# Kernel optimization log

Measured on AMD Instinct MI355X. Metric: run time of the kernel, lower is better.

Reference implementation:

```python
import jax, jax.numpy as jnp
import numpy as np

D_MODEL = 256
HIDDEN = 64
R = 1            # corr_radius
MAX_DELTA = 4.0  # max_delta_px
GROUPS = 8       # _gn_groups(64)
B, H, W = 2, 128, 128


def grid_sample_border(img, grid):
    """Bilinear grid_sample, padding_mode='border', align_corners=False.
    img: [B,C,H,W], grid: [B,Hg,Wg,2] (x,y in [-1,1]-ish). -> [B,C,Hg,Wg]"""
    Bi, C, Hi, Wi = img.shape
    x = (grid[..., 0] + 1.0) * (Wi * 0.5) - 0.5
    y = (grid[..., 1] + 1.0) * (Hi * 0.5) - 0.5
    x = jnp.clip(x, 0.0, Wi - 1.0)
    y = jnp.clip(y, 0.0, Hi - 1.0)
    x0 = jnp.floor(x); y0 = jnp.floor(y)
    wx = (x - x0)[:, None]; wy = (y - y0)[:, None]
    x0i = x0.astype(jnp.int32); y0i = y0.astype(jnp.int32)
    x1i = jnp.minimum(x0i + 1, Wi - 1); y1i = jnp.minimum(y0i + 1, Hi - 1)
    imgf = img.reshape(Bi, C, Hi * Wi)
    def gat(im, yi, xi):  # im [C,HW], yi/xi [Hg,Wg]
        return im[:, (yi * Wi + xi).reshape(-1)].reshape(C, *yi.shape)
    g = jax.vmap(gat)
    v00 = g(imgf, y0i, x0i); v01 = g(imgf, y0i, x1i)
    v10 = g(imgf, y1i, x0i); v11 = g(imgf, y1i, x1i)
    return (v00 * (1 - wx) * (1 - wy) + v01 * wx * (1 - wy)
            + v10 * (1 - wx) * wy + v11 * wx * wy)


def l2norm(x, axis):
    n = jnp.sqrt(jnp.sum(x * x, axis=axis, keepdims=True))
    return x / jnp.maximum(n, 1e-12)


def conv2d(x, w, pad):
    return jax.lax.conv_general_dilated(x, w, (1, 1), [(pad, pad), (pad, pad)],
                                        dimension_numbers=('NCHW', 'OIHW', 'NCHW'))


def group_norm(x, gamma, beta, groups=GROUPS, eps=1e-5):
    Bi, C, Hi, Wi = x.shape
    xg = x.reshape(Bi, groups, C // groups, Hi, Wi)
    mu = xg.mean(axis=(2, 3, 4), keepdims=True)
    var = xg.var(axis=(2, 3, 4), keepdims=True)
    xn = ((xg - mu) * jax.lax.rsqrt(var + eps)).reshape(Bi, C, Hi, Wi)
    return xn * gamma[None, :, None, None] + beta[None, :, None, None]


def conv_gn_gelu(x, w, g, b, pad):
    return jax.nn.gelu(group_norm(conv2d(x, w, pad), g, b), approximate=False)


def make_grid(h, w):
    xs = (jnp.arange(w, dtype=jnp.float32) + 0.5) * (2.0 / w) - 1.0
    ys = (jnp.arange(h, dtype=jnp.float32) + 0.5) * (2.0 / h) - 1.0
    gx, gy = jnp.meshgrid(xs, ys, indexing='xy')
    return jnp.stack([gx, gy], axis=-1)[None]  # [1,H,W,2]


def setup_inputs() -> dict:
    key = jax.random.key(0)
    ks = jax.random.split(key, 12)
    in_ch = D_MODEL * 3 + 2 + 1 + (2 * R + 1) ** 2  # 780
    def w(k, o, i, kh, kw):
        return (jax.random.normal(k, (o, i, kh, kw), jnp.float32)
                / np.sqrt(i * kh * kw).astype(np.float32))
    return {
        'feat_A_map': jax.random.normal(ks[0], (B, D_MODEL, H, W), jnp.float32),
        'feat_B_map': jax.random.normal(ks[1], (B, D_MODEL, H, W), jnp.float32),
        'coarse_warp': jax.random.uniform(ks[2], (B, H, W, 2), jnp.float32, -1.0, 1.0),
        'confidence': jax.random.uniform(ks[3], (B, H, W), jnp.float32),
        'enc1_w': w(ks[4], HIDDEN, in_ch, 1, 1),
        'gn1_g': jnp.ones(HIDDEN, jnp.float32), 'gn1_b': jnp.zeros(HIDDEN, jnp.float32),
        'enc2_w': w(ks[5], HIDDEN, HIDDEN, 3, 3),
        'gn2_g': jnp.ones(HIDDEN, jnp.float32), 'gn2_b': jnp.zeros(HIDDEN, jnp.float32),
        'enc3_w': w(ks[6], HIDDEN, HIDDEN, 3, 3),
        'gn3_g': jnp.ones(HIDDEN, jnp.float32), 'gn3_b': jnp.zeros(HIDDEN, jnp.float32),
        'delta_w': w(ks[7], 2, HIDDEN, 3, 3) * 0.01, 'delta_b': jnp.zeros(2, jnp.float32),
        'conf_w': w(ks[8], 1, HIDDEN, 3, 3) * 0.01, 'conf_b': jnp.zeros(1, jnp.float32),
    }


def reference(feat_A_map, feat_B_map, coarse_warp, confidence,
              enc1_w, gn1_g, gn1_b, enc2_w, gn2_g, gn2_b, enc3_w, gn3_g, gn3_b,
              delta_w, delta_b, conf_w, conf_b):
    cw = jnp.clip(jnp.nan_to_num(coarse_warp, nan=0.0, posinf=1.5, neginf=-1.5), -1.5, 1.5)
    route = jax.lax.stop_gradient(cw)  # detached routing warp
    warped_B = grid_sample_border(feat_B_map, route)
    src = make_grid(H, W)
    disp = jnp.transpose(cw - src, (0, 3, 1, 2))  # [B,2,H,W]
    conf = jnp.clip(jnp.nan_to_num(confidence, nan=0.0, posinf=1.0, neginf=0.0), 0.0, 1.0)
    conf_chw = conf[:, None]
    # warp-aware correlation over (2R+1)^2 offsets, vectorized via vmap
    fa_n = l2norm(jnp.nan_to_num(feat_A_map, nan=0.0, posinf=0.0, neginf=0.0), axis=1)
    fb = jnp.nan_to_num(feat_B_map, nan=0.0, posinf=0.0, neginf=0.0)
    offs = jnp.asarray([[2.0 * dx / W, 2.0 * dy / H]
                        for dy in range(-R, R + 1) for dx in range(-R, R + 1)],
                       dtype=jnp.float32)  # [K,2]
    grids = jnp.clip(jnp.nan_to_num(route[None] + offs[:, None, None, None, :],
                                    nan=0.0, posinf=1.5, neginf=-1.5), -1.5, 1.5)
    sampled = jax.vmap(grid_sample_border, in_axes=(None, 0))(fb, grids)  # [K,B,C,H,W]
    corr = jnp.transpose(jnp.sum(fa_n[None] * l2norm(sampled, axis=2), axis=2),
                         (1, 0, 2, 3))  # [B,K,H,W]
    x = jnp.concatenate([feat_A_map, warped_B, jnp.abs(feat_A_map - warped_B),
                         disp, conf_chw, corr], axis=1)
    h = conv_gn_gelu(x, enc1_w, gn1_g, gn1_b, 0)
    h = conv_gn_gelu(h, enc2_w, gn2_g, gn2_b, 1)
    h = conv_gn_gelu(h, enc3_w, gn3_g, gn3_b, 1)
    delta_raw = jnp.transpose(jnp.tanh(conv2d(h, delta_w, 1)
                                       + delta_b[None, :, None, None]), (0, 2, 3, 1))
    scale = jnp.asarray([2.0 * MAX_DELTA / W, 2.0 * MAX_DELTA / H], jnp.float32)
    fine_warp = jnp.clip(jnp.nan_to_num(route + delta_raw * scale,
                                        nan=0.0, posinf=1.5, neginf=-1.5), -1.5, 1.5)
    conf_delta = (conv2d(h, conf_w, 1) + conf_b[None, :, None, None])[:, 0]
    p = jnp.clip(conf, 1e-4, 1.0 - 1e-4)
    base_logit = jnp.log(p) - jnp.log1p(-p)
    refined_logits = base_logit + 0.5 * conf_delta
    refined_conf = jnp.clip(jax.nn.sigmoid(refined_logits), 0.0, 1.0)
    return (fine_warp, refined_conf, refined_logits)
```

## Files before the change

kernel.cpp:

```cpp
#include <hip/hip_runtime.h>
#include <hip/hip_bf16.h>
#include <math.h>

#define B_ 2
#define H_ 128
#define W_ 128
#define C_ 256
#define HID 64
#define PIX_PER (H_*W_)
#define NPIX (B_*PIX_PER)
#define K1STEPS 25
#define K3STEPS 18

using f32x4 = __attribute__((ext_vector_type(4))) float;
using s16x8 = __attribute__((ext_vector_type(8))) short;
using u16x2 = __attribute__((ext_vector_type(2))) unsigned short;
using u16x4 = __attribute__((ext_vector_type(4))) unsigned short;
using u16x8 = __attribute__((ext_vector_type(8))) unsigned short;

__device__ __forceinline__ float bf2f(unsigned short u) {
    return __uint_as_float(((unsigned)u) << 16);
}
__device__ __forceinline__ unsigned short f2bf(float f) {
    unsigned u = __float_as_uint(f);
    u += 0x7FFFu + ((u >> 16) & 1u);
    return (unsigned short)(u >> 16);
}
__device__ __forceinline__ float clean15(float v) {
    if (v != v) v = 0.f;
    return fminf(fmaxf(v, -1.5f), 1.5f);
}
__device__ __forceinline__ float clean01(float v) {
    if (v != v) v = 0.f;
    return fminf(fmaxf(v, 0.f), 1.f);
}

__global__ __launch_bounds__(256) void k_transpose(const float* __restrict__ A,
                                                   const float* __restrict__ Bm,
                                                   unsigned short* __restrict__ faT,
                                                   unsigned short* __restrict__ fbT)
{
    __shared__ float tile[32][33];
    int hw0 = blockIdx.x * 32;
    int c0  = blockIdx.y * 32;
    int z   = blockIdx.z;
    int b   = z >> 1;
    const float* src = (z & 1) ? Bm : A;
    unsigned short* dst = (z & 1) ? fbT : faT;
    int tx = threadIdx.x & 31, ty = threadIdx.x >> 5;
    const float* s = src + ((size_t)b * C_ + c0) * (size_t)PIX_PER + hw0;
#pragma unroll
    for (int i = 0; i < 32; i += 8) {
        float v = s[(size_t)(ty + i) * PIX_PER + tx];
        if (!isfinite(v)) v = 0.f;
        tile[ty + i][tx] = v;
    }
    __syncthreads();
    unsigned short* d = dst + ((size_t)b * PIX_PER + hw0) * C_ + c0;
#pragma unroll
    for (int i = 0; i < 32; i += 8) {
        int hwl = ty + i;
        u16x2 o;
        o[0] = f2bf(tile[2 * tx][hwl]);
        o[1] = f2bf(tile[2 * tx + 1][hwl]);
        *(u16x2*)(d + (size_t)hwl * C_ + 2 * tx) = o;
    }
}

__global__ __launch_bounds__(256) void k_pack(const float* __restrict__ w1,
                                              const float* __restrict__ w2,
                                              const float* __restrict__ w3,
                                              unsigned short* __restrict__ p1,
                                              unsigned short* __restrict__ p2,
                                              unsigned short* __restrict__ p3)
{
    int t = blockIdx.x * 256 + threadIdx.x;
    if (t < 6400) {
        int lane = t & 63, nt = (t >> 6) & 3, ks = t >> 8;
        int n = nt * 16 + (lane & 15);
        int kb = ks * 32 + 8 * (lane >> 4);
#pragma unroll
        for (int j = 0; j < 8; j++) {
            int k = kb + j;
            p1[(size_t)t * 8 + j] = (k < 780) ? f2bf(w1[(size_t)n * 780 + k]) : (unsigned short)0;
        }
    } else if (t < 6400 + 2 * 4608) {
        int which = (t - 6400) / 4608;
        int idx = (t - 6400) % 4608;
        const float* w = which ? w3 : w2;
        unsigned short* p = which ? p3 : p2;
        int lane = idx & 63, nt = (idx >> 6) & 3, ks = idx >> 8;
        int n = nt * 16 + (lane & 15);
        int tap = ks >> 1;
        int ky = tap / 3, kx = tap % 3;
#pragma unroll
        for (int j = 0; j < 8; j++) {
            int c = (ks & 1) * 32 + 8 * (lane >> 4) + j;
            p[(size_t)idx * 8 + j] = f2bf(w[(((size_t)n * 64 + c) * 3 + ky) * 3 + kx]);
        }
    }
}

__global__ __launch_bounds__(256, 4) void k_sample(const float* __restrict__ cw,
                                                   const float* __restrict__ confp,
                                                   const unsigned short* __restrict__ faT,
                                                   const unsigned short* __restrict__ fbT,
                                                   unsigned short* __restrict__ wbbuf,
                                                   unsigned short* __restrict__ tail)
{
    int wid = (blockIdx.x * 256 + threadIdx.x) >> 6;
    int lane = threadIdx.x & 63;
    int b = wid >> 14, y = (wid >> 7) & 127, x = wid & 127;

    float gx = clean15(cw[(size_t)wid * 2 + 0]);
    float gy = clean15(cw[(size_t)wid * 2 + 1]);

    float pxu = (gx + 1.f) * 64.f - 0.5f;
    float pyu = (gy + 1.f) * 64.f - 0.5f;
    float x0f = floorf(pxu), y0f = floorf(pyu);
    float wx = pxu - x0f, wy = pyu - y0f;
    int x0 = (int)x0f, y0 = (int)y0f;
    int cx[4], cy[4];
#pragma unroll
    for (int k = 0; k < 4; k++) {
        cx[k] = min(max(x0 - 1 + k, 0), 127);
        cy[k] = min(max(y0 - 1 + k, 0), 127);
    }

    const unsigned short* fbB = fbT + (size_t)b * PIX_PER * C_ + lane * 4;
    u16x4 tp[4][4];
#pragma unroll
    for (int m = 0; m < 4; m++)
#pragma unroll
        for (int k = 0; k < 4; k++)
            tp[m][k] = *(const u16x4*)(fbB + (size_t)(cy[m] * 128 + cx[k]) * C_);

    float fa[4], fa2 = 0.f;
    {
        u16x4 v = *(const u16x4*)(faT + (size_t)wid * C_ + lane * 4);
#pragma unroll
        for (int i = 0; i < 4; i++) { fa[i] = bf2f(v[i]); fa2 += fa[i] * fa[i]; }
    }

    float A[4][3], P[4][3], Q[3][3], rxp[3][4], wbv[4];
#pragma unroll
    for (int r = 0; r < 4; r++) {
        float rx[3][4];
#pragma unroll
        for (int dx = 0; dx < 3; dx++)
#pragma unroll
            for (int i = 0; i < 4; i++) {
                float t0 = bf2f(tp[r][dx][i]);
                float t1 = bf2f(tp[r][dx + 1][i]);
                rx[dx][i] = t0 + wx * (t1 - t0);
            }
#pragma unroll
        for (int dx = 0; dx < 3; dx++) {
            float a = 0.f, p = 0.f;
#pragma unroll
            for (int i = 0; i < 4; i++) { a += fa[i] * rx[dx][i]; p += rx[dx][i] * rx[dx][i]; }
            A[r][dx] = a; P[r][dx] = p;
            if (r > 0) {
                float q = 0.f;
#pragma unroll
                for (int i = 0; i < 4; i++) q += rxp[dx][i] * rx[dx][i];
                Q[r - 1][dx] = q;
            }
        }
        if (r == 1) {
#pragma unroll
            for (int i = 0; i < 4; i++) wbv[i] = rx[1][i];
        }
        if (r == 2) {
#pragma unroll
            for (int i = 0; i < 4; i++) wbv[i] += wy * (rx[1][i] - wbv[i]);
        }
        if (r < 3) {
#pragma unroll
            for (int dx = 0; dx < 3; dx++)
#pragma unroll
                for (int i = 0; i < 4; i++) rxp[dx][i] = rx[dx][i];
        }
    }

    u16x4 wbo;
#pragma unroll
    for (int i = 0; i < 4; i++) wbo[i] = f2bf(wbv[i]);
    *(u16x4*)(wbbuf + (size_t)wid * C_ + lane * 4) = wbo;

    float red[19];
    float u0 = (1.f - wy) * (1.f - wy), u1 = 2.f * wy * (1.f - wy), u2 = wy * wy;
#pragma unroll
    for (int j = 0; j < 9; j++) {
        int dy = j / 3, dx = j % 3;
        red[j]     = A[dy][dx] + wy * (A[dy + 1][dx] - A[dy][dx]);
        red[9 + j] = u0 * P[dy][dx] + u1 * Q[dy][dx] + u2 * P[dy + 1][dx];
    }
    red[18] = fa2;
#pragma unroll
    for (int m = 1; m < 64; m <<= 1)
#pragma unroll
        for (int j = 0; j < 19; j++)
            red[j] += __shfl_xor(red[j], m);

    if (lane == 0) {
        float conf = clean01(confp[wid]);
        float inv_na = rsqrtf(fmaxf(red[18], 1e-24f));
        float srcx = ((float)x + 0.5f) * 0.015625f - 1.f;
        float srcy = ((float)y + 0.5f) * 0.015625f - 1.f;
        u16x8 t0, t1, tz;
        t0[0] = f2bf(gx - srcx);
        t0[1] = f2bf(gy - srcy);
        t0[2] = f2bf(conf);
#pragma unroll
        for (int j = 0; j < 5; j++)
            t0[3 + j] = f2bf(red[j] * inv_na * rsqrtf(fmaxf(red[9 + j], 1e-24f)));
#pragma unroll
        for (int j = 0; j < 4; j++)
            t1[j] = f2bf(red[5 + j] * inv_na * rsqrtf(fmaxf(red[14 + j], 1e-24f)));
#pragma unroll
        for (int j = 4; j < 8; j++) t1[j] = 0;
#pragma unroll
        for (int j = 0; j < 8; j++) tz[j] = 0;
        unsigned short* tr = tail + (size_t)wid * 32;
        *(u16x8*)(tr)      = t0;
        *(u16x8*)(tr + 8)  = t1;
        *(u16x8*)(tr + 16) = tz;
        *(u16x8*)(tr + 24) = tz;
    }
}

__device__ __forceinline__ void gn_epilogue(const f32x4 acc[4], float* lds,
                                            float* __restrict__ pbuf, int bid,
                                            int la, int lb, int wv)
{
    int d = la >> 3;
    int slot = wv * 32 + lb * 8 + (la & 7);
#pragma unroll
    for (int nt = 0; nt < 4; nt++) {
        float s  = acc[nt][0] + acc[nt][1] + acc[nt][2] + acc[nt][3];
        float s2 = acc[nt][0] * acc[nt][0] + acc[nt][1] * acc[nt][1]
                 + acc[nt][2] * acc[nt][2] + acc[nt][3] * acc[nt][3];
        int g = nt * 2 + d;
        lds[(g * 128 + slot) * 2 + 0] = s;
        lds[(g * 128 + slot) * 2 + 1] = s2;
    }
    __syncthreads();
    int tid = threadIdx.x;
    int g = tid >> 5, i = tid & 31;
    float s  = lds[(g * 128 + i) * 2]     + lds[(g * 128 + i + 32) * 2]
             + lds[(g * 128 + i + 64) * 2] + lds[(g * 128 + i + 96) * 2];
    float s2 = lds[(g * 128 + i) * 2 + 1]     + lds[(g * 128 + i + 32) * 2 + 1]
             + lds[(g * 128 + i + 64) * 2 + 1] + lds[(g * 128 + i + 96) * 2 + 1];
#pragma unroll
    for (int m = 1; m < 32; m <<= 1) { s += __shfl_xor(s, m); s2 += __shfl_xor(s2, m); }
    if (i == 0) {
        pbuf[(bid * 8 + g) * 2]     = s;
        pbuf[(bid * 8 + g) * 2 + 1] = s2;
    }
}

__global__ __launch_bounds__(256) void k_gemm1(const unsigned short* __restrict__ faT,
                                               const unsigned short* __restrict__ wbbuf,
                                               const unsigned short* __restrict__ tail,
                                               const unsigned short* __restrict__ pack,
                                               unsigned short* __restrict__ hpre,
                                               float* __restrict__ pbuf)
{
    __shared__ float lds[8 * 128 * 2];
    int wave = (blockIdx.x * 256 + threadIdx.x) >> 6;
    int lane = threadIdx.x & 63;
    int la = lane & 15, lb = lane >> 4;
    int row = wave * 16 + la;
    const unsigned short* fa_row = faT   + (size_t)row * C_ + lb * 8;
    const unsigned short* wb_row = wbbuf + (size_t)row * C_ + lb * 8;
    f32x4 acc[4] = {{0,0,0,0},{0,0,0,0},{0,0,0,0},{0,0,0,0}};

#pragma unroll
    for (int ks = 0; ks < 8; ks++) {
        s16x8 a = *(const s16x8*)(fa_row + ks * 32);
#pragma unroll
        for (int nt = 0; nt < 4; nt++)
            acc[nt] = __builtin_amdgcn_mfma_f32_16x16x32_bf16(a,
                *(const s16x8*)(pack + ((size_t)(ks * 4 + nt) * 64 + lane) * 8), acc[nt], 0, 0, 0);
    }
#pragma unroll
    for (int ks = 0; ks < 8; ks++) {
        s16x8 a = *(const s16x8*)(wb_row + ks * 32);
#pragma unroll
        for (int nt = 0; nt < 4; nt++)
            acc[nt] = __builtin_amdgcn_mfma_f32_16x16x32_bf16(a,
                *(const s16x8*)(pack + ((size_t)((ks + 8) * 4 + nt) * 64 + lane) * 8), acc[nt], 0, 0, 0);
    }
#pragma unroll
    for (int ks = 0; ks < 8; ks++) {
        u16x8 av = *(const u16x8*)(fa_row + ks * 32);
        u16x8 bv = *(const u16x8*)(wb_row + ks * 32);
        s16x8 a;
#pragma unroll
        for (int j = 0; j < 8; j++)
            a[j] = (short)f2bf(fabsf(bf2f(av[j]) - bf2f(bv[j])));
#pragma unroll
        for (int nt = 0; nt < 4; nt++)
            acc[nt] = __builtin_amdgcn_mfma_f32_16x16x32_bf16(a,
                *(const s16x8*)(pack + ((size_t)((ks + 16) * 4 + nt) * 64 + lane) * 8), acc[nt], 0, 0, 0);
    }
    {
        s16x8 a = *(const s16x8*)(tail + (size_t)row * 32 + lb * 8);
#pragma unroll
        for (int nt = 0; nt < 4; nt++)
            acc[nt] = __builtin_amdgcn_mfma_f32_16x16x32_bf16(a,
                *(const s16x8*)(pack + ((size_t)(24 * 4 + nt) * 64 + lane) * 8), acc[nt], 0, 0, 0);
    }

    int orow = wave * 16 + lb * 4;
#pragma unroll
    for (int nt = 0; nt < 4; nt++)
#pragma unroll
        for (int r = 0; r < 4; r++)
            hpre[(size_t)(orow + r) * HID + nt * 16 + la] = f2bf(acc[nt][r]);

    gn_epilogue(acc, lds, pbuf, blockIdx.x, la, lb, (threadIdx.x >> 6));
}

__global__ __launch_bounds__(256) void k_conv3(const unsigned short* __restrict__ hin,
                                               const unsigned short* __restrict__ pack,
                                               unsigned short* __restrict__ hpre,
                                               float* __restrict__ pbuf)
{
    __shared__ float lds[8 * 128 * 2];
    int wave = (blockIdx.x * 256 + threadIdx.x) >> 6;
    int lane = threadIdx.x & 63;
    int la = lane & 15, lb = lane >> 4;
    int b = wave >> 10, y = (wave >> 3) & 127, xb = (wave & 7) * 16;
    int xx = xb + la;
    f32x4 acc[4] = {{0,0,0,0},{0,0,0,0},{0,0,0,0},{0,0,0,0}};
#pragma unroll
    for (int ks = 0; ks < K3STEPS; ks++) {
        int tap = ks >> 1;
        int yy = y + tap / 3 - 1;
        int xq = xx + tap % 3 - 1;
        s16x8 a = {0,0,0,0,0,0,0,0};
        if ((unsigned)yy < 128u && (unsigned)xq < 128u)
            a = *(const s16x8*)(hin + ((size_t)((b * 128 + yy) * 128 + xq)) * HID
                                + (ks & 1) * 32 + lb * 8);
#pragma unroll
        for (int nt = 0; nt < 4; nt++)
            acc[nt] = __builtin_amdgcn_mfma_f32_16x16x32_bf16(a,
                *(const s16x8*)(pack + ((size_t)(ks * 4 + nt) * 64 + lane) * 8), acc[nt], 0, 0, 0);
    }
    int orow = wave * 16 + lb * 4;
#pragma unroll
    for (int nt = 0; nt < 4; nt++)
#pragma unroll
        for (int r = 0; r < 4; r++)
            hpre[(size_t)(orow + r) * HID + nt * 16 + la] = f2bf(acc[nt][r]);

    gn_epilogue(acc, lds, pbuf, blockIdx.x, la, lb, (threadIdx.x >> 6));
}

__global__ __launch_bounds__(256) void k_gnapply(const unsigned short* __restrict__ hpre,
                                                 const float* __restrict__ gamma,
                                                 const float* __restrict__ beta,
                                                 const float* __restrict__ pbuf,
                                                 unsigned short* __restrict__ hn)
{
    int pix0 = blockIdx.x * 32;
    int b = pix0 >> 14;
    __shared__ float sm[16];
    {
        int g = threadIdx.x >> 5, i = threadIdx.x & 31;
        float s = 0.f, s2 = 0.f;
#pragma unroll
        for (int k = 0; k < 8; k++) {
            int bid = b * 256 + i + k * 32;
            s  += pbuf[(bid * 8 + g) * 2];
            s2 += pbuf[(bid * 8 + g) * 2 + 1];
        }
#pragma unroll
        for (int m = 1; m < 32; m <<= 1) { s += __shfl_xor(s, m); s2 += __shfl_xor(s2, m); }
        if (i == 0) {
            const float inv = 1.f / 131072.f;
            float mean = s * inv;
            float var = fmaxf(s2 * inv - mean * mean, 0.f);
            sm[g * 2] = mean;
            sm[g * 2 + 1] = rsqrtf(var + 1e-5f);
        }
    }
    __syncthreads();
    int t = blockIdx.x * 256 + threadIdx.x;
    int pix = t >> 3, g = t & 7;
    float mean = sm[g * 2], rstd = sm[g * 2 + 1];
    u16x8 v = *(const u16x8*)(hpre + (size_t)pix * HID + g * 8);
    u16x8 o;
#pragma unroll
    for (int i = 0; i < 8; i++) {
        int c = g * 8 + i;
        float xn = (bf2f(v[i]) - mean) * rstd * gamma[c] + beta[c];
        float ge = 0.5f * xn * (1.f + erff(xn * 0.70710678118654752f));
        o[i] = f2bf(ge);
    }
    *(u16x8*)(hn + (size_t)pix * HID + g * 8) = o;
}

__global__ __launch_bounds__(256) void k_final(const unsigned short* __restrict__ hn,
                                               const float* __restrict__ cw,
                                               const float* __restrict__ confp,
                                               const float* __restrict__ dw,
                                               const float* __restrict__ db,
                                               const float* __restrict__ cwgt,
                                               const float* __restrict__ cb,
                                               float* __restrict__ out)
{
    __shared__ float wds[1154];
    __shared__ float wcs[577];
    int tid = threadIdx.x;
    for (int i = tid; i < 1152; i += 256) wds[i] = dw[i];
    for (int i = tid; i < 576; i += 256) wcs[i] = cwgt[i];
    if (tid == 0) { wds[1152] = db[0]; wds[1153] = db[1]; wcs[576] = cb[0]; }
    __syncthreads();

    int t = blockIdx.x * 256 + tid;
    int pix = t >> 3, part = t & 7;
    int b = pix >> 14, y = (pix >> 7) & 127, x = pix & 127;

    float d0 = 0.f, d1 = 0.f, c0 = 0.f;
#pragma unroll
    for (int ky = 0; ky < 3; ky++) {
        int yy = y + ky - 1;
        if ((unsigned)yy >= 128u) continue;
#pragma unroll
        for (int kx = 0; kx < 3; kx++) {
            int xq = x + kx - 1;
            if ((unsigned)xq >= 128u) continue;
            const unsigned short* hp = hn + (size_t)((b * 128 + yy) * 128 + xq) * HID + part * 8;
            int widx = ky * 3 + kx;
            u16x8 v = *(const u16x8*)hp;
#pragma unroll
            for (int i = 0; i < 8; i++) {
                float f = bf2f(v[i]);
                int c = part * 8 + i;
                d0 += f * wds[c * 9 + widx];
                d1 += f * wds[576 + c * 9 + widx];
                c0 += f * wcs[c * 9 + widx];
            }
        }
    }
#pragma unroll
    for (int m = 1; m < 8; m <<= 1) {
        d0 += __shfl_xor(d0, m);
        d1 += __shfl_xor(d1, m);
        c0 += __shfl_xor(c0, m);
    }
    if (part == 0) {
        d0 = tanhf(d0 + wds[1152]);
        d1 = tanhf(d1 + wds[1153]);
        c0 += wcs[576];

        float gx = clean15(cw[(size_t)pix * 2 + 0]);
        float gy = clean15(cw[(size_t)pix * 2 + 1]);
        float fwx = fminf(fmaxf(gx + d0 * 0.0625f, -1.5f), 1.5f);
        float fwy = fminf(fmaxf(gy + d1 * 0.0625f, -1.5f), 1.5f);

        float conf = clean01(confp[pix]);
        float p = fminf(fmaxf(conf, 1e-4f), 1.f - 1e-4f);
        float bl = logf(p) - log1pf(-p);
        float rl = bl + 0.5f * c0;
        float rc = fminf(fmaxf(1.f / (1.f + expf(-rl)), 0.f), 1.f);

        out[(size_t)pix * 2 + 0] = fwx;
        out[(size_t)pix * 2 + 1] = fwy;
        out[(size_t)NPIX * 2 + pix] = rc;
        out[(size_t)NPIX * 2 + NPIX + pix] = rl;
    }
}

extern "C" void kernel_launch(void* const* d_in, const int* in_sizes, int n_in,
                              void* d_out, int out_size, void* d_ws, size_t ws_size,
                              hipStream_t stream)
{
    const float* feat_A = (const float*)d_in[0];
    const float* feat_B = (const float*)d_in[1];
    const float* cw     = (const float*)d_in[2];
    const float* conf   = (const float*)d_in[3];
    const float* w1     = (const float*)d_in[4];
    const float* g1     = (const float*)d_in[5];
    const float* b1     = (const float*)d_in[6];
    const float* w2     = (const float*)d_in[7];
    const float* g2     = (const float*)d_in[8];
    const float* b2     = (const float*)d_in[9];
    const float* w3     = (const float*)d_in[10];
    const float* g3     = (const float*)d_in[11];
    const float* b3     = (const float*)d_in[12];
    const float* dw     = (const float*)d_in[13];
    const float* db     = (const float*)d_in[14];
    const float* cwgt   = (const float*)d_in[15];
    const float* cb     = (const float*)d_in[16];
    float* out = (float*)d_out;

    char* w = (char*)d_ws;
    size_t o = 0;
    unsigned short* faT  = (unsigned short*)(w + o); o += (size_t)NPIX * C_ * 2;
    unsigned short* fbT  = (unsigned short*)(w + o); o += (size_t)NPIX * C_ * 2;
    unsigned short* wbb  = (unsigned short*)(w + o); o += (size_t)NPIX * C_ * 2;
    unsigned short* tail = (unsigned short*)(w + o); o += (size_t)NPIX * 32 * 2;
    unsigned short* hpre = (unsigned short*)(w + o); o += (size_t)NPIX * HID * 2;
    unsigned short* hnA  = (unsigned short*)(w + o); o += (size_t)NPIX * HID * 2;
    unsigned short* hnB  = (unsigned short*)(w + o); o += (size_t)NPIX * HID * 2;
    unsigned short* p1   = (unsigned short*)(w + o); o += (size_t)K1STEPS * 4 * 64 * 8 * 2;
    unsigned short* p2   = (unsigned short*)(w + o); o += (size_t)K3STEPS * 4 * 64 * 8 * 2;
    unsigned short* p3   = (unsigned short*)(w + o); o += (size_t)K3STEPS * 4 * 64 * 8 * 2;
    float* pbuf = (float*)(w + o);

    k_transpose<<<dim3(PIX_PER / 32, C_ / 32, 4), 256, 0, stream>>>(feat_A, feat_B, faT, fbT);
    k_pack<<<61, 256, 0, stream>>>(w1, w2, w3, p1, p2, p3);
    k_sample<<<NPIX / 4, 256, 0, stream>>>(cw, conf, faT, fbT, wbb, tail);

    k_gemm1<<<(NPIX / 16) / 4, 256, 0, stream>>>(faT, wbb, tail, p1, hpre, pbuf);
    k_gnapply<<<NPIX / 32, 256, 0, stream>>>(hpre, g1, b1, pbuf, hnA);

    k_conv3<<<(NPIX / 16) / 4, 256, 0, stream>>>(hnA, p2, hpre, pbuf);
    k_gnapply<<<NPIX / 32, 256, 0, stream>>>(hpre, g2, b2, pbuf, hnB);

    k_conv3<<<(NPIX / 16) / 4, 256, 0, stream>>>(hnB, p3, hpre, pbuf);
    k_gnapply<<<NPIX / 32, 256, 0, stream>>>(hpre, g3, b3, pbuf, hnA);

    k_final<<<NPIX * 8 / 256, 256, 0, stream>>>(hnA, cw, conf, dw, db, cwgt, cb, out);
}
```

Measured before the change: 151.7 us.

## Process two pixels per wave in k_sample with 16-byte loads and packed math

k_sample now assigns each pixel to a half-wave of 32 lanes instead of a full 64-lane wave, so each lane handles 8 channels through 16-byte loads instead of 4 channels through 8-byte loads. The bilinear interpolation and dot products use float2 vectors so the compiler can emit packed FP32 ops. Taps are loaded one row at a time to limit register pressure, and the shuffle reduction drops one step. The grid is halved and the occupancy hint in launch_bounds is removed, which may change register allocation and occupancy.

```diff
diff --git a/kernel.cpp b/kernel.cpp
--- a/kernel.cpp
+++ b/kernel.cpp
@@ -12,11 +12,13 @@
 #define K1STEPS 25
 #define K3STEPS 18
 
+using f32x2 = __attribute__((ext_vector_type(2))) float;
 using f32x4 = __attribute__((ext_vector_type(4))) float;
 using s16x8 = __attribute__((ext_vector_type(8))) short;
 using u16x2 = __attribute__((ext_vector_type(2))) unsigned short;
 using u16x4 = __attribute__((ext_vector_type(4))) unsigned short;
 using u16x8 = __attribute__((ext_vector_type(8))) unsigned short;
+using u32x4 = __attribute__((ext_vector_type(4))) unsigned int;
 
 __device__ __forceinline__ float bf2f(unsigned short u) {
     return __uint_as_float(((unsigned)u) << 16);
@@ -33,6 +35,15 @@
 __device__ __forceinline__ float clean01(float v) {
     if (v != v) v = 0.f;
     return fminf(fmaxf(v, 0.f), 1.f);
+}
+__device__ __forceinline__ void cvt8(u32x4 v, f32x2* o) {
+#pragma unroll
+    for (int p = 0; p < 4; p++) {
+        f32x2 t;
+        t.x = __uint_as_float(v[p] << 16);
+        t.y = __uint_as_float(v[p] & 0xffff0000u);
+        o[p] = t;
+    }
 }
 
 __global__ __launch_bounds__(256) void k_transpose(const float* __restrict__ A,
@@ -101,15 +112,17 @@
     }
 }
 
-__global__ __launch_bounds__(256, 4) void k_sample(const float* __restrict__ cw,
-                                                   const float* __restrict__ confp,
-                                                   const unsigned short* __restrict__ faT,
-                                                   const unsigned short* __restrict__ fbT,
-                                                   unsigned short* __restrict__ wbbuf,
-                                                   unsigned short* __restrict__ tail)
-{
-    int wid = (blockIdx.x * 256 + threadIdx.x) >> 6;
+__global__ __launch_bounds__(256) void k_sample(const float* __restrict__ cw,
+                                                const float* __restrict__ confp,
+                                                const unsigned short* __restrict__ faT,
+                                                const unsigned short* __restrict__ fbT,
+                                                unsigned short* __restrict__ wbbuf,
+                                                unsigned short* __restrict__ tail)
+{
     int lane = threadIdx.x & 63;
+    int wave = (blockIdx.x * 256 + threadIdx.x) >> 6;
+    int sub = lane & 31;
+    int wid = wave * 2 + (lane >> 5);
     int b = wid >> 14, y = (wid >> 7) & 127, x = wid & 127;
 
     float gx = clean15(cw[(size_t)wid * 2 + 0]);
@@ -120,73 +133,73 @@
     float x0f = floorf(pxu), y0f = floorf(pyu);
     float wx = pxu - x0f, wy = pyu - y0f;
     int x0 = (int)x0f, y0 = (int)y0f;
-    int cx[4], cy[4];
+    int co[4], ro[4];
 #pragma unroll
     for (int k = 0; k < 4; k++) {
-        cx[k] = min(max(x0 - 1 + k, 0), 127);
-        cy[k] = min(max(y0 - 1 + k, 0), 127);
-    }
-
-    const unsigned short* fbB = fbT + (size_t)b * PIX_PER * C_ + lane * 4;
-    u16x4 tp[4][4];
-#pragma unroll
-    for (int m = 0; m < 4; m++)
+        co[k] = min(max(x0 - 1 + k, 0), 127) << 8;
+        ro[k] = min(max(y0 - 1 + k, 0), 127) << 15;
+    }
+    const unsigned short* fbB = fbT + ((size_t)b << 22) + sub * 8;
+    const f32x2 wx2 = {wx, wx};
+
+    f32x2 fav[4];
+    cvt8(*(const u32x4*)(faT + (size_t)wid * C_ + sub * 8), fav);
+    f32x2 fa2v = fav[0]*fav[0] + fav[1]*fav[1] + fav[2]*fav[2] + fav[3]*fav[3];
+    float fa2 = fa2v.x + fa2v.y;
+
+    float A[4][3], P[4][3], Q[3][3];
+    f32x2 rxp[3][4];
+    f32x2 wbv[4];
+
+#pragma unroll
+    for (int r = 0; r < 4; r++) {
+        u32x4 tp[4];
 #pragma unroll
         for (int k = 0; k < 4; k++)
-            tp[m][k] = *(const u16x4*)(fbB + (size_t)(cy[m] * 128 + cx[k]) * C_);
-
-    float fa[4], fa2 = 0.f;
-    {
-        u16x4 v = *(const u16x4*)(faT + (size_t)wid * C_ + lane * 4);
-#pragma unroll
-        for (int i = 0; i < 4; i++) { fa[i] = bf2f(v[i]); fa2 += fa[i] * fa[i]; }
-    }
-
-    float A[4][3], P[4][3], Q[3][3], rxp[3][4], wbv[4];
-#pragma unroll
-    for (int r = 0; r < 4; r++) {
-        float rx[3][4];
-#pragma unroll
-        for (int dx = 0; dx < 3; dx++)
+            tp[k] = *(const u32x4*)(fbB + ro[r] + co[k]);
+        f32x2 e0[4], e1[4];
+        cvt8(tp[0], e0);
+#pragma unroll
+        for (int dx = 0; dx < 3; dx++) {
+            cvt8(tp[dx + 1], e1);
+            f32x2 rx[4];
+            f32x2 a = {0.f, 0.f}, p = {0.f, 0.f};
 #pragma unroll
             for (int i = 0; i < 4; i++) {
-                float t0 = bf2f(tp[r][dx][i]);
-                float t1 = bf2f(tp[r][dx + 1][i]);
-                rx[dx][i] = t0 + wx * (t1 - t0);
+                rx[i] = e0[i] + wx2 * (e1[i] - e0[i]);
+                a += fav[i] * rx[i];
+                p += rx[i] * rx[i];
             }
-#pragma unroll
-        for (int dx = 0; dx < 3; dx++) {
-            float a = 0.f, p = 0.f;
-#pragma unroll
-            for (int i = 0; i < 4; i++) { a += fa[i] * rx[dx][i]; p += rx[dx][i] * rx[dx][i]; }
-            A[r][dx] = a; P[r][dx] = p;
+            A[r][dx] = a.x + a.y;
+            P[r][dx] = p.x + p.y;
             if (r > 0) {
-                float q = 0.f;
-#pragma unroll
-                for (int i = 0; i < 4; i++) q += rxp[dx][i] * rx[dx][i];
-                Q[r - 1][dx] = q;
+                f32x2 q = rxp[dx][0]*rx[0] + rxp[dx][1]*rx[1]
+                        + rxp[dx][2]*rx[2] + rxp[dx][3]*rx[3];
+                Q[r - 1][dx] = q.x + q.y;
             }
+            if (dx == 1) {
+                if (r == 1) {
+#pragma unroll
+                    for (int i = 0; i < 4; i++) wbv[i] = rx[i];
+                }
+                if (r == 2) {
+                    f32x2 wy2 = {wy, wy};
+#pragma unroll
+                    for (int i = 0; i < 4; i++) wbv[i] += wy2 * (rx[i] - wbv[i]);
+                }
+            }
+#pragma unroll
+            for (int i = 0; i < 4; i++) { rxp[dx][i] = rx[i]; e0[i] = e1[i]; }
         }
-        if (r == 1) {
-#pragma unroll
-            for (int i = 0; i < 4; i++) wbv[i] = rx[1][i];
-        }
-        if (r == 2) {
-#pragma unroll
-            for (int i = 0; i < 4; i++) wbv[i] += wy * (rx[1][i] - wbv[i]);
-        }
-        if (r < 3) {
-#pragma unroll
-            for (int dx = 0; dx < 3; dx++)
-#pragma unroll
-                for (int i = 0; i < 4; i++) rxp[dx][i] = rx[dx][i];
-        }
-    }
-
-    u16x4 wbo;
-#pragma unroll
-    for (int i = 0; i < 4; i++) wbo[i] = f2bf(wbv[i]);
-    *(u16x4*)(wbbuf + (size_t)wid * C_ + lane * 4) = wbo;
+    }
+
+    u16x8 wbo;
+#pragma unroll
+    for (int i = 0; i < 4; i++) {
+        wbo[2 * i]     = f2bf(wbv[i].x);
+        wbo[2 * i + 1] = f2bf(wbv[i].y);
+    }
+    *(u16x8*)(wbbuf + (size_t)wid * C_ + sub * 8) = wbo;
 
     float red[19];
     float u0 = (1.f - wy) * (1.f - wy), u1 = 2.f * wy * (1.f - wy), u2 = wy * wy;
@@ -198,12 +211,12 @@
     }
     red[18] = fa2;
 #pragma unroll
-    for (int m = 1; m < 64; m <<= 1)
+    for (int m = 1; m < 32; m <<= 1)
 #pragma unroll
         for (int j = 0; j < 19; j++)
             red[j] += __shfl_xor(red[j], m);
 
-    if (lane == 0) {
+    if (sub == 0) {
         float conf = clean01(confp[wid]);
         float inv_na = rsqrtf(fmaxf(red[18], 1e-24f));
         float srcx = ((float)x + 0.5f) * 0.015625f - 1.f;
@@ -514,7 +527,7 @@
 
     k_transpose<<<dim3(PIX_PER / 32, C_ / 32, 4), 256, 0, stream>>>(feat_A, feat_B, faT, fbT);
     k_pack<<<61, 256, 0, stream>>>(w1, w2, w3, p1, p2, p3);
-    k_sample<<<NPIX / 4, 256, 0, stream>>>(cw, conf, faT, fbT, wbb, tail);
+    k_sample<<<NPIX / 8, 256, 0, stream>>>(cw, conf, faT, fbT, wbb, tail);
 
     k_gemm1<<<(NPIX / 16) / 4, 256, 0, stream>>>(faT, wbb, tail, p1, hpre, pbuf);
     k_gnapply<<<NPIX / 32, 256, 0, stream>>>(hpre, g1, b1, pbuf, hnA);
```

Result: faster. 138.9 us (-8.4%).

## Compute correlation via MFMA Gram matrix of sampled taps and fuse weight packing

Applied to the files above, without the earlier changes.

The sampling kernel now builds a 16x16 Gram matrix with bf16 MFMA. It covers the query feature and the 4x4 neighbourhood taps. Each bilinear correlation and its norm is then assembled from Gram entries, so the 19 separate wave reductions are no longer needed. The weight-packing kernel is folded into the transpose launch as an extra grid slice to save a launch, and the transpose store pattern is reshaped. The risk is extra LDS traffic, plus a small numeric change from the expanded norm formula, which could lose accuracy to cancellation.

```diff
diff --git a/kernel.cpp b/kernel.cpp
--- a/kernel.cpp
+++ b/kernel.cpp
@@ -12,6 +12,7 @@
 #define K1STEPS 25
 #define K3STEPS 18
 
+using f32x2 = __attribute__((ext_vector_type(2))) float;
 using f32x4 = __attribute__((ext_vector_type(4))) float;
 using s16x8 = __attribute__((ext_vector_type(8))) short;
 using u16x2 = __attribute__((ext_vector_type(2))) unsigned short;
@@ -38,8 +39,43 @@
 __global__ __launch_bounds__(256) void k_transpose(const float* __restrict__ A,
                                                    const float* __restrict__ Bm,
                                                    unsigned short* __restrict__ faT,
-                                                   unsigned short* __restrict__ fbT)
-{
+                                                   unsigned short* __restrict__ fbT,
+                                                   const float* __restrict__ w1,
+                                                   const float* __restrict__ w2,
+                                                   const float* __restrict__ w3,
+                                                   unsigned short* __restrict__ p1,
+                                                   unsigned short* __restrict__ p2,
+                                                   unsigned short* __restrict__ p3)
+{
+    if (blockIdx.z == 4) {
+        if (blockIdx.y != 0 || blockIdx.x >= 61) return;
+        int t = blockIdx.x * 256 + threadIdx.x;
+        if (t < 6400) {
+            int lane = t & 63, nt = (t >> 6) & 3, ks = t >> 8;
+            int n = nt * 16 + (lane & 15);
+            int kb = ks * 32 + 8 * (lane >> 4);
+#pragma unroll
+            for (int j = 0; j < 8; j++) {
+                int k = kb + j;
+                p1[(size_t)t * 8 + j] = (k < 780) ? f2bf(w1[(size_t)n * 780 + k]) : (unsigned short)0;
+            }
+        } else if (t < 6400 + 2 * 4608) {
+            int which = (t - 6400) / 4608;
+            int idx = (t - 6400) % 4608;
+            const float* w = which ? w3 : w2;
+            unsigned short* p = which ? p3 : p2;
+            int lane = idx & 63, nt = (idx >> 6) & 3, ks = idx >> 8;
+            int n = nt * 16 + (lane & 15);
+            int tap = ks >> 1;
+            int ky = tap / 3, kx = tap % 3;
+#pragma unroll
+            for (int j = 0; j < 8; j++) {
+                int c = (ks & 1) * 32 + 8 * (lane >> 4) + j;
+                p[(size_t)idx * 8 + j] = f2bf(w[(((size_t)n * 64 + c) * 3 + ky) * 3 + kx]);
+            }
+        }
+        return;
+    }
     __shared__ float tile[32][33];
     int hw0 = blockIdx.x * 32;
     int c0  = blockIdx.y * 32;
@@ -57,176 +93,124 @@
     }
     __syncthreads();
     unsigned short* d = dst + ((size_t)b * PIX_PER + hw0) * C_ + c0;
-#pragma unroll
-    for (int i = 0; i < 32; i += 8) {
-        int hwl = ty + i;
+    int pr = threadIdx.x & 15;
+    int hw = threadIdx.x >> 4;
+#pragma unroll
+    for (int i = 0; i < 32; i += 16) {
+        int hwl = hw + i;
         u16x2 o;
-        o[0] = f2bf(tile[2 * tx][hwl]);
-        o[1] = f2bf(tile[2 * tx + 1][hwl]);
-        *(u16x2*)(d + (size_t)hwl * C_ + 2 * tx) = o;
-    }
-}
-
-__global__ __launch_bounds__(256) void k_pack(const float* __restrict__ w1,
-                                              const float* __restrict__ w2,
-                                              const float* __restrict__ w3,
-                                              unsigned short* __restrict__ p1,
-                                              unsigned short* __restrict__ p2,
-                                              unsigned short* __restrict__ p3)
-{
-    int t = blockIdx.x * 256 + threadIdx.x;
-    if (t < 6400) {
-        int lane = t & 63, nt = (t >> 6) & 3, ks = t >> 8;
-        int n = nt * 16 + (lane & 15);
-        int kb = ks * 32 + 8 * (lane >> 4);
-#pragma unroll
-        for (int j = 0; j < 8; j++) {
-            int k = kb + j;
-            p1[(size_t)t * 8 + j] = (k < 780) ? f2bf(w1[(size_t)n * 780 + k]) : (unsigned short)0;
-        }
-    } else if (t < 6400 + 2 * 4608) {
-        int which = (t - 6400) / 4608;
-        int idx = (t - 6400) % 4608;
-        const float* w = which ? w3 : w2;
-        unsigned short* p = which ? p3 : p2;
-        int lane = idx & 63, nt = (idx >> 6) & 3, ks = idx >> 8;
-        int n = nt * 16 + (lane & 15);
-        int tap = ks >> 1;
-        int ky = tap / 3, kx = tap % 3;
-#pragma unroll
-        for (int j = 0; j < 8; j++) {
-            int c = (ks & 1) * 32 + 8 * (lane >> 4) + j;
-            p[(size_t)idx * 8 + j] = f2bf(w[(((size_t)n * 64 + c) * 3 + ky) * 3 + kx]);
-        }
-    }
-}
-
-__global__ __launch_bounds__(256, 4) void k_sample(const float* __restrict__ cw,
-                                                   const float* __restrict__ confp,
-                                                   const unsigned short* __restrict__ faT,
-                                                   const unsigned short* __restrict__ fbT,
-                                                   unsigned short* __restrict__ wbbuf,
-                                                   unsigned short* __restrict__ tail)
-{
-    int wid = (blockIdx.x * 256 + threadIdx.x) >> 6;
+        o[0] = f2bf(tile[2 * pr][hwl]);
+        o[1] = f2bf(tile[2 * pr + 1][hwl]);
+        *(u16x2*)(d + (size_t)hwl * C_ + 2 * pr) = o;
+    }
+}
+
+__global__ __launch_bounds__(256) void k_sample(const float* __restrict__ cw,
+                                                const float* __restrict__ confp,
+                                                const unsigned short* __restrict__ faT,
+                                                const unsigned short* __restrict__ fbT,
+                                                unsigned short* __restrict__ wbbuf,
+                                                unsigned short* __restrict__ tail)
+{
+    __shared__ float CT[4][16 * 20 + 4];
     int lane = threadIdx.x & 63;
+    int wv = threadIdx.x >> 6;
+    int wid = blockIdx.x * 4 + wv;
     int b = wid >> 14, y = (wid >> 7) & 127, x = wid & 127;
 
     float gx = clean15(cw[(size_t)wid * 2 + 0]);
     float gy = clean15(cw[(size_t)wid * 2 + 1]);
+    float conf = clean01(confp[wid]);
 
     float pxu = (gx + 1.f) * 64.f - 0.5f;
     float pyu = (gy + 1.f) * 64.f - 0.5f;
     float x0f = floorf(pxu), y0f = floorf(pyu);
     float wx = pxu - x0f, wy = pyu - y0f;
     int x0 = (int)x0f, y0 = (int)y0f;
-    int cx[4], cy[4];
-#pragma unroll
-    for (int k = 0; k < 4; k++) {
-        cx[k] = min(max(x0 - 1 + k, 0), 127);
-        cy[k] = min(max(y0 - 1 + k, 0), 127);
-    }
-
-    const unsigned short* fbB = fbT + (size_t)b * PIX_PER * C_ + lane * 4;
-    u16x4 tp[4][4];
-#pragma unroll
-    for (int m = 0; m < 4; m++)
-#pragma unroll
-        for (int k = 0; k < 4; k++)
-            tp[m][k] = *(const u16x4*)(fbB + (size_t)(cy[m] * 128 + cx[k]) * C_);
-
-    float fa[4], fa2 = 0.f;
-    {
-        u16x4 v = *(const u16x4*)(faT + (size_t)wid * C_ + lane * 4);
-#pragma unroll
-        for (int i = 0; i < 4; i++) { fa[i] = bf2f(v[i]); fa2 += fa[i] * fa[i]; }
-    }
-
-    float A[4][3], P[4][3], Q[3][3], rxp[3][4], wbv[4];
-#pragma unroll
-    for (int r = 0; r < 4; r++) {
-        float rx[3][4];
-#pragma unroll
-        for (int dx = 0; dx < 3; dx++)
-#pragma unroll
-            for (int i = 0; i < 4; i++) {
-                float t0 = bf2f(tp[r][dx][i]);
-                float t1 = bf2f(tp[r][dx + 1][i]);
-                rx[dx][i] = t0 + wx * (t1 - t0);
-            }
-#pragma unroll
-        for (int dx = 0; dx < 3; dx++) {
-            float a = 0.f, p = 0.f;
-#pragma unroll
-            for (int i = 0; i < 4; i++) { a += fa[i] * rx[dx][i]; p += rx[dx][i] * rx[dx][i]; }
-            A[r][dx] = a; P[r][dx] = p;
-            if (r > 0) {
-                float q = 0.f;
-#pragma unroll
-                for (int i = 0; i < 4; i++) q += rxp[dx][i] * rx[dx][i];
-                Q[r - 1][dx] = q;
-            }
+    int co0 = min(max(x0 - 1, 0), 127) << 8;
+    int co1 = min(max(x0    , 0), 127) << 8;
+    int co2 = min(max(x0 + 1, 0), 127) << 8;
+    int co3 = min(max(x0 + 2, 0), 127) << 8;
+    int ro0 = min(max(y0 - 1, 0), 127) << 15;
+    int ro1 = min(max(y0    , 0), 127) << 15;
+    int ro2 = min(max(y0 + 1, 0), 127) << 15;
+    int ro3 = min(max(y0 + 2, 0), 127) << 15;
+
+    const unsigned short* fbP = fbT + ((size_t)b << 22);
+
+    int q = lane & 15;
+    int ta = q - 1;
+    int tA = max(ta, 0);
+    int myA = tA >> 2, mxA = tA & 3;
+    int roA = myA == 0 ? ro0 : myA == 1 ? ro1 : myA == 2 ? ro2 : ro3;
+    int coA = mxA == 0 ? co0 : mxA == 1 ? co1 : mxA == 2 ? co2 : co3;
+    int myB = q >> 2, mxB = q & 3;
+    int roB = myB == 0 ? ro0 : myB == 1 ? ro1 : myB == 2 ? ro2 : ro3;
+    int coB = mxB == 0 ? co0 : mxB == 1 ? co1 : mxB == 2 ? co2 : co3;
+    int chunk = (lane >> 4) * 8;
+    const unsigned short* baseA = (ta < 0) ? (faT + (size_t)wid * C_ + chunk)
+                                           : (fbP + roA + coA + chunk);
+    const unsigned short* baseB = fbP + roB + coB + chunk;
+
+    f32x4 acc = {0.f, 0.f, 0.f, 0.f};
+#pragma unroll
+    for (int ks = 0; ks < 8; ks++) {
+        s16x8 av = *(const s16x8*)(baseA + ks * 32);
+        s16x8 bv = *(const s16x8*)(baseB + ks * 32);
+        acc = __builtin_amdgcn_mfma_f32_16x16x32_bf16(av, bv, acc, 0, 0, 0);
+    }
+    *(f32x4*)&CT[wv][(lane & 15) * 20 + (lane >> 4) * 4] = acc;
+
+    float w00 = (1.f - wx) * (1.f - wy), w01 = wx * (1.f - wy);
+    float w10 = (1.f - wx) * wy,         w11 = wx * wy;
+    u16x4 v5  = *(const u16x4*)(fbP + ro1 + co1 + lane * 4);
+    u16x4 v6  = *(const u16x4*)(fbP + ro1 + co2 + lane * 4);
+    u16x4 v9  = *(const u16x4*)(fbP + ro2 + co1 + lane * 4);
+    u16x4 v10 = *(const u16x4*)(fbP + ro2 + co2 + lane * 4);
+    u16x4 v15 = *(const u16x4*)(fbP + ro3 + co3 + lane * 4);
+    u16x4 vfa = *(const u16x4*)(faT + (size_t)wid * C_ + lane * 4);
+    float fa2p = 0.f, t152p = 0.f;
+    u16x4 wbo;
+#pragma unroll
+    for (int i = 0; i < 4; i++) {
+        float s = w00 * bf2f(v5[i]) + w01 * bf2f(v6[i])
+                + w10 * bf2f(v9[i]) + w11 * bf2f(v10[i]);
+        wbo[i] = f2bf(s);
+        float fv = bf2f(vfa[i]), tv = bf2f(v15[i]);
+        fa2p  += fv * fv;
+        t152p += tv * tv;
+    }
+    *(u16x4*)(wbbuf + (size_t)wid * C_ + lane * 4) = wbo;
+#pragma unroll
+    for (int m = 1; m < 64; m <<= 1) {
+        fa2p  += __shfl_xor(fa2p, m);
+        t152p += __shfl_xor(t152p, m);
+    }
+
+    if (lane < 32) {
+        float outv = 0.f;
+        if (lane == 0)      outv = gx - (((float)x + 0.5f) * 0.015625f - 1.f);
+        else if (lane == 1) outv = gy - (((float)y + 0.5f) * 0.015625f - 1.f);
+        else if (lane == 2) outv = conf;
+        else if (lane < 12) {
+            int j = lane - 3;
+            int jd = j / 3, jm = j - jd * 3;
+            int m00 = jd * 4 + jm;
+            const float* Cw = &CT[wv][0];
+            float D00 = Cw[m00 * 20], D01 = Cw[(m00 + 1) * 20];
+            float D10 = Cw[(m00 + 4) * 20], D11 = Cw[(m00 + 5) * 20];
+            float dot = w00 * D00 + w01 * D01 + w10 * D10 + w11 * D11;
+#define GR(a, b) Cw[(b) * 20 + (a) + 1]
+            float g11 = (j == 8) ? t152p : GR(m00 + 5, m00 + 5);
+            float s2 = w00 * w00 * GR(m00, m00) + w01 * w01 * GR(m00 + 1, m00 + 1)
+                     + w10 * w10 * GR(m00 + 4, m00 + 4) + w11 * w11 * g11
+                     + 2.f * (w00 * w01 * GR(m00, m00 + 1) + w00 * w10 * GR(m00, m00 + 4)
+                            + w00 * w11 * GR(m00, m00 + 5) + w01 * w10 * GR(m00 + 1, m00 + 4)
+                            + w01 * w11 * GR(m00 + 1, m00 + 5) + w10 * w11 * GR(m00 + 4, m00 + 5));
+#undef GR
+            outv = dot * rsqrtf(fmaxf(fa2p, 1e-24f)) * rsqrtf(fmaxf(s2, 1e-24f));
         }
-        if (r == 1) {
-#pragma unroll
-            for (int i = 0; i < 4; i++) wbv[i] = rx[1][i];
-        }
-        if (r == 2) {
-#pragma unroll
-            for (int i = 0; i < 4; i++) wbv[i] += wy * (rx[1][i] - wbv[i]);
-        }
-        if (r < 3) {
-#pragma unroll
-            for (int dx = 0; dx < 3; dx++)
-#pragma unroll
-                for (int i = 0; i < 4; i++) rxp[dx][i] = rx[dx][i];
-        }
-    }
-
-    u16x4 wbo;
-#pragma unroll
-    for (int i = 0; i < 4; i++) wbo[i] = f2bf(wbv[i]);
-    *(u16x4*)(wbbuf + (size_t)wid * C_ + lane * 4) = wbo;
-
-    float red[19];
-    float u0 = (1.f - wy) * (1.f - wy), u1 = 2.f * wy * (1.f - wy), u2 = wy * wy;
-#pragma unroll
-    for (int j = 0; j < 9; j++) {
-        int dy = j / 3, dx = j % 3;
-        red[j]     = A[dy][dx] + wy * (A[dy + 1][dx] - A[dy][dx]);
-        red[9 + j] = u0 * P[dy][dx] + u1 * Q[dy][dx] + u2 * P[dy + 1][dx];
-    }
-    red[18] = fa2;
-#pragma unroll
-    for (int m = 1; m < 64; m <<= 1)
-#pragma unroll
-        for (int j = 0; j < 19; j++)
-            red[j] += __shfl_xor(red[j], m);
-
-    if (lane == 0) {
-        float conf = clean01(confp[wid]);
-        float inv_na = rsqrtf(fmaxf(red[18], 1e-24f));
-        float srcx = ((float)x + 0.5f) * 0.015625f - 1.f;
-        float srcy = ((float)y + 0.5f) * 0.015625f - 1.f;
-        u16x8 t0, t1, tz;
-        t0[0] = f2bf(gx - srcx);
-        t0[1] = f2bf(gy - srcy);
-        t0[2] = f2bf(conf);
-#pragma unroll
-        for (int j = 0; j < 5; j++)
-            t0[3 + j] = f2bf(red[j] * inv_na * rsqrtf(fmaxf(red[9 + j], 1e-24f)));
-#pragma unroll
-        for (int j = 0; j < 4; j++)
-            t1[j] = f2bf(red[5 + j] * inv_na * rsqrtf(fmaxf(red[14 + j], 1e-24f)));
-#pragma unroll
-        for (int j = 4; j < 8; j++) t1[j] = 0;
-#pragma unroll
-        for (int j = 0; j < 8; j++) tz[j] = 0;
-        unsigned short* tr = tail + (size_t)wid * 32;
-        *(u16x8*)(tr)      = t0;
-        *(u16x8*)(tr + 8)  = t1;
-        *(u16x8*)(tr + 16) = tz;
-        *(u16x8*)(tr + 24) = tz;
+        tail[(size_t)wid * 32 + lane] = f2bf(outv);
     }
 }
 
@@ -512,8 +496,8 @@
     unsigned short* p3   = (unsigned short*)(w + o); o += (size_t)K3STEPS * 4 * 64 * 8 * 2;
     float* pbuf = (float*)(w + o);
 
-    k_transpose<<<dim3(PIX_PER / 32, C_ / 32, 4), 256, 0, stream>>>(feat_A, feat_B, faT, fbT);
-    k_pack<<<61, 256, 0, stream>>>(w1, w2, w3, p1, p2, p3);
+    k_transpose<<<dim3(PIX_PER / 32, C_ / 32, 5), 256, 0, stream>>>(feat_A, feat_B, faT, fbT,
+                                                                    w1, w2, w3, p1, p2, p3);
     k_sample<<<NPIX / 4, 256, 0, stream>>>(cw, conf, faT, fbT, wbb, tail);
 
     k_gemm1<<<(NPIX / 16) / 4, 256, 0, stream>>>(faT, wbb, tail, p1, hpre, pbuf);
```

Result: slower. 170.9 us (+12.7%).
